# Optimization experiments

Measured on AMD Instinct MI355X. Metric: run time of the kernel, lower is better.

The kernel has to match this reference:

```python
import jax, jax.numpy as jnp
import numpy as np

V, D, N, T, U, E = 200000, 128, 50000, 20, 128, 128

def setup_inputs() -> dict:
    key = jax.random.key(0)
    ks = jax.random.split(key, 12)
    s = 0.02
    return {
        "node_ids": jax.random.randint(ks[0], (N,), 0, V, dtype=jnp.int32),
        "neigh_ids": jax.random.randint(ks[1], (N, T), 0, V, dtype=jnp.int32),
        "alpha": jax.random.uniform(ks[2], (N, T), dtype=jnp.float32),
        "table": jax.random.normal(ks[3], (V, D), dtype=jnp.float32),
        "Wq": jax.random.normal(ks[4], (D, U), dtype=jnp.float32) * s,
        "bq": jnp.zeros((U,), dtype=jnp.float32),
        "Wn": jax.random.normal(ks[5], (D, U), dtype=jnp.float32) * s,
        "bn": jnp.zeros((U,), dtype=jnp.float32),
        "Ww": jax.random.normal(ks[6], (2 * U, U), dtype=jnp.float32) * s,
        "bw": jnp.zeros((U,), dtype=jnp.float32),
        "Wg": jax.random.normal(ks[7], (U, E), dtype=jnp.float32) * s,
        "bg": jnp.zeros((E,), dtype=jnp.float32),
    }

def reference(node_ids, neigh_ids, alpha, table, Wq, bq, Wn, bn, Ww, bw, Wg, bg):
    # gather initial embeddings (irregular indexing)
    node_x = table[node_ids]            # [N, D]
    neigh_x = table[neigh_ids]          # [N, T, D]
    # Convolve: node branch Dense+ReLU
    node_h = jax.nn.relu(node_x @ Wq + bq)                       # [N, U]
    # Aggregator: neighbor Dense+ReLU then alpha-weighted matmul
    neigh_h = jax.nn.relu(jnp.einsum('ntd,du->ntu', neigh_x, Wn) + bn)  # [N, T, U]
    agg = jnp.einsum('nt,ntu->nu', alpha, neigh_h)               # [N, U]
    # concat + Dense+ReLU
    emb = jax.nn.relu(jnp.concatenate([node_h, agg], axis=-1) @ Ww + bw)  # [N, U]
    # global (Frobenius) L2 normalize, as in tf.divide(Emb, tf.norm(Emb, ord=2))
    emb = emb / jnp.linalg.norm(emb)
    # final Dense+ReLU to emb_dim
    return jax.nn.relu(emb @ Wg + bg)                            # [N, E]
```

## Files before the change

kernel.cpp:

```cpp
#include <hip/hip_runtime.h>
#include <math.h>


using f32x4  = __attribute__((ext_vector_type(4))) float;
using short8 = __attribute__((ext_vector_type(8))) short;

typedef const void __attribute__((address_space(1))) gvoid_t;
typedef void       __attribute__((address_space(3))) svoid_t;

__device__ __forceinline__ void gload16(const void* g, void* l) {
    __builtin_amdgcn_global_load_lds((gvoid_t*)g, (svoid_t*)l, 16, 0, 0);
}

__device__ __forceinline__ ushort f2bf(float f) {
    uint u = __float_as_uint(f);
    return (ushort)((u + 0x7fffu + ((u >> 16) & 1u)) >> 16);
}
__device__ __forceinline__ float bf2f(ushort h) {
    return __uint_as_float((uint)h << 16);
}
__device__ __forceinline__ uint pk2(float lo, float hi) {
    return (uint)f2bf(lo) | ((uint)f2bf(hi) << 16);
}
__device__ __forceinline__ short8 pack8(f32x4 a, f32x4 b) {
    uint4 r;
    r.x = pk2(a[0], a[1]); r.y = pk2(a[2], a[3]);
    r.z = pk2(b[0], b[1]); r.w = pk2(b[2], b[3]);
    union { uint4 u; short8 s; } cv; cv.u = r; return cv.s;
}

__global__ __launch_bounds__(256)
void prep_weights(const float* __restrict__ Wq, const float* __restrict__ Wn,
                  const float* __restrict__ Ww, const float* __restrict__ Wg,
                  ushort* __restrict__ WqT, ushort* __restrict__ WnT,
                  ushort* __restrict__ WwT, ushort* __restrict__ WgT)
{
    int idx = blockIdx.x * 256 + threadIdx.x;
    const float* W; ushort* WT; int K; int j = idx;
    if (j < 16384)      { W = Wq; WT = WqT; K = 128; }
    else if (j < 32768) { W = Wn; WT = WnT; K = 128; j -= 16384; }
    else if (j < 65536) { W = Ww; WT = WwT; K = 256; j -= 32768; }
    else                { W = Wg; WT = WgT; K = 128; j -= 65536; }
    int n = j & 127, k = j >> 7;
    WT[(size_t)n * K + k] = f2bf(W[j]);
}

template<bool GATHER>
__device__ __forceinline__ void stage_tile(const float* __restrict__ table,
                                           const int* __restrict__ gidx,
                                           float* Ab, int tile, int M,
                                           int w, int l)
{
#pragma unroll
    for (int j = 0; j < 8; ++j) {
        const int u   = j * 2 + w;
        const int idx = u * 64 + l;
        const int r   = idx >> 5;
        const int c   = idx & 31;
        int grow = tile * 32 + r;
        if (grow > M - 1) grow = M - 1;
        const int g = GATHER ? gidx[grow] : grow;
        const char* src = (const char*)table + (size_t)g * 512
                        + (size_t)((c * 16) ^ ((r & 7) << 4));
        gload16(src, (char*)Ab + u * 1024);
    }
}

__global__ __launch_bounds__(128, 2)
void k1_async(const float* __restrict__ table, const int* __restrict__ node_ids,
              const ushort* __restrict__ WnT, const float* __restrict__ bn,
              const ushort* __restrict__ WqT, const float* __restrict__ bq,
              ushort* __restrict__ H, ushort* __restrict__ nh,
              int V, int N, int splitH)
{
    __shared__ __align__(16) ushort Wlds[128 * 128];
    __shared__ __align__(16) float  Abuf[2][32 * 128];
    __shared__ __align__(16) float  blds[128];
    const int tid = threadIdx.x;
    const int w = tid >> 6, l = tid & 63, l16 = l & 15, lh = l >> 4;
    const bool isH = (int)blockIdx.x < splitH;

    const ushort* WT = isH ? WnT : WqT;
#pragma unroll
    for (int it = 0; it < 16; ++it) {
        int idx = it * 128 + tid, n = idx >> 4, o = idx & 15;
        uint4 v = *reinterpret_cast<const uint4*>(&WT[(size_t)n * 128 + 8 * o]);
        *reinterpret_cast<uint4*>((char*)Wlds + n * 256 + ((16 * o) ^ ((n & 7) << 4))) = v;
    }
    blds[tid] = (isH ? bn : bq)[tid];

    const int M   = isH ? V : N;
    ushort* out   = isH ? H : nh;
    const int ldo = isH ? 128 : 256;
    const int nt  = (M + 31) >> 5;
    const int bidx = isH ? (int)blockIdx.x : (int)blockIdx.x - splitH;
    const int nblk = isH ? splitH : (int)gridDim.x - splitH;

    int tile = bidx;
    if (tile < nt) {
        if (isH) stage_tile<false>(table, nullptr,  Abuf[0], tile, M, w, l);
        else     stage_tile<true >(table, node_ids, Abuf[0], tile, M, w, l);
    }
    __syncthreads();

    int cur = 0;
    const int r = 16 * w + l16;
    for (; tile < nt; tile += nblk) {
        const int nxt = tile + nblk;
        if (nxt < nt) {
            if (isH) stage_tile<false>(table, nullptr,  Abuf[cur ^ 1], nxt, M, w, l);
            else     stage_tile<true >(table, node_ids, Abuf[cur ^ 1], nxt, M, w, l);
        }

        const char* Ab = (const char*)Abuf[cur];
        short8 a[4];
#pragma unroll
        for (int ks = 0; ks < 4; ++ks) {
            f32x4 b0 = *reinterpret_cast<const f32x4*>(
                Ab + r * 512 + ((ks * 128 + lh * 32)      ^ ((r & 7) << 4)));
            f32x4 b1 = *reinterpret_cast<const f32x4*>(
                Ab + r * 512 + ((ks * 128 + lh * 32 + 16) ^ ((r & 7) << 4)));
            a[ks] = pack8(b0, b1);
        }

        f32x4 acc[8];
#pragma unroll
        for (int mt = 0; mt < 8; ++mt)
#pragma unroll
            for (int i = 0; i < 4; ++i) acc[mt][i] = 0.f;
#pragma unroll
        for (int ks = 0; ks < 4; ++ks)
#pragma unroll
            for (int mt = 0; mt < 8; ++mt) {
                short8 wf = *reinterpret_cast<const short8*>(
                    (const char*)Wlds + (16 * mt + l16) * 256 +
                    ((64 * ks + 16 * lh) ^ ((l16 & 7) << 4)));
                acc[mt] = __builtin_amdgcn_mfma_f32_16x16x32_bf16(wf, a[ks], acc[mt], 0, 0, 0);
            }

        const int grow = tile * 32 + r;
        if (grow < M) {
#pragma unroll
            for (int mt = 0; mt < 8; ++mt) {
                f32x4 bv = *reinterpret_cast<const f32x4*>(&blds[16 * mt + 4 * lh]);
                uint2 q;
                q.x = pk2(fmaxf(acc[mt][0] + bv[0], 0.f), fmaxf(acc[mt][1] + bv[1], 0.f));
                q.y = pk2(fmaxf(acc[mt][2] + bv[2], 0.f), fmaxf(acc[mt][3] + bv[3], 0.f));
                *reinterpret_cast<uint2*>(&out[(size_t)grow * ldo + 16 * mt + 4 * lh]) = q;
            }
        }
        __syncthreads();
        cur ^= 1;
    }
}

__global__ __launch_bounds__(256)
void agg_bf16(const ushort* __restrict__ H,
              const int* __restrict__ nids,
              const float* __restrict__ alpha,
              ushort* __restrict__ outb,
              int N)
{
    const int n   = blockIdx.x * 16 + (threadIdx.x >> 4);
    const int l16 = threadIdx.x & 15;
    if (n >= N) return;

    const int*   idp = &nids[n * 20];
    const float* alp = &alpha[n * 20];
    float a[8];
#pragma unroll
    for (int j = 0; j < 8; ++j) a[j] = 0.f;
#pragma unroll
    for (int t = 0; t < 20; ++t) {
        const int   id = idp[t];
        const float al = alp[t];
        uint4 h = *reinterpret_cast<const uint4*>(&H[(size_t)id * 128 + 8 * l16]);
        a[0] = fmaf(al, bf2f((ushort)(h.x & 0xffff)), a[0]);
        a[1] = fmaf(al, bf2f((ushort)(h.x >> 16)),    a[1]);
        a[2] = fmaf(al, bf2f((ushort)(h.y & 0xffff)), a[2]);
        a[3] = fmaf(al, bf2f((ushort)(h.y >> 16)),    a[3]);
        a[4] = fmaf(al, bf2f((ushort)(h.z & 0xffff)), a[4]);
        a[5] = fmaf(al, bf2f((ushort)(h.z >> 16)),    a[5]);
        a[6] = fmaf(al, bf2f((ushort)(h.w & 0xffff)), a[6]);
        a[7] = fmaf(al, bf2f((ushort)(h.w >> 16)),    a[7]);
    }
    uint4 p;
    p.x = pk2(a[0], a[1]); p.y = pk2(a[2], a[3]);
    p.z = pk2(a[4], a[5]); p.w = pk2(a[6], a[7]);
    *reinterpret_cast<uint4*>(&outb[(size_t)n * 256 + 8 * l16]) = p;
}

template<int KTOT, bool GATHER, bool ABF16, bool SUMSQ, bool SCALE, bool OUTBF16>
__global__ __launch_bounds__(256, 2)
void mfma_gemm(const void* __restrict__ Av, int lda,
               const int* __restrict__ gidx,
               const ushort* __restrict__ WT,
               const float* __restrict__ bias,
               void* __restrict__ outv, int ldo, int M,
               float* __restrict__ partials,
               const float* __restrict__ scale_ptr)
{
    __shared__ __align__(16) char smem[65536];
    __shared__ float red[256];
    char* Bbase = smem + 32768;

    const int tid = threadIdx.x;
    const int w   = tid >> 6;
    const int l   = tid & 63;
    const int l16 = l & 15, lh = l >> 4;
    const int brow = blockIdx.x * 128;

    f32x4 acc[2][8];
#pragma unroll
    for (int fr = 0; fr < 2; ++fr)
#pragma unroll
        for (int fc = 0; fc < 8; ++fc)
#pragma unroll
            for (int i = 0; i < 4; ++i) acc[fr][fc][i] = 0.f;

    for (int k0 = 0; k0 < KTOT; k0 += 128) {
        if (ABF16) {
            const ushort* A = (const ushort*)Av;
#pragma unroll
            for (int it = 0; it < 8; ++it) {
                int idx = it * 256 + tid;
                int r = idx >> 4, o = idx & 15;
                int row = brow + r; int grow = (row < M) ? row : (M - 1);
                if (GATHER) grow = gidx[grow];
                uint4 v = *reinterpret_cast<const uint4*>(&A[(size_t)grow * lda + k0 + 8 * o]);
                *reinterpret_cast<uint4*>(smem + r * 256 + ((16 * o) ^ ((r & 7) << 4))) = v;
            }
        } else {
            const float* A = (const float*)Av;
#pragma unroll
            for (int it = 0; it < 16; ++it) {
                int idx = it * 256 + tid;
                int r = idx >> 5, q = idx & 31;
                int row = brow + r; int grow = (row < M) ? row : (M - 1);
                if (GATHER) grow = gidx[grow];
                float4 v = *reinterpret_cast<const float4*>(&A[(size_t)grow * lda + k0 + 4 * q]);
                uint2 p;
                p.x = pk2(v.x, v.y);
                p.y = pk2(v.z, v.w);
                *reinterpret_cast<uint2*>(smem + r * 256 + ((8 * q) ^ ((r & 7) << 4))) = p;
            }
        }
#pragma unroll
        for (int it = 0; it < 8; ++it) {
            int idx = it * 256 + tid;
            int n = idx >> 4, o = idx & 15;
            uint4 v = *reinterpret_cast<const uint4*>(&WT[(size_t)n * KTOT + k0 + 8 * o]);
            *reinterpret_cast<uint4*>(Bbase + n * 256 + ((16 * o) ^ ((n & 7) << 4))) = v;
        }
        __syncthreads();

        const int r0 = 32 * w + l16;
        const int r1 = r0 + 16;
#pragma unroll
        for (int ks = 0; ks < 4; ++ks) {
            const int kb = 64 * ks + 16 * lh;
            short8 a0 = *reinterpret_cast<const short8*>(
                smem + r0 * 256 + (kb ^ ((r0 & 7) << 4)));
            short8 a1 = *reinterpret_cast<const short8*>(
                smem + r1 * 256 + (kb ^ ((r1 & 7) << 4)));
#pragma unroll
            for (int fc = 0; fc < 8; ++fc) {
                const int nn = 16 * fc + l16;
                short8 b = *reinterpret_cast<const short8*>(
                    Bbase + nn * 256 + (kb ^ ((nn & 7) << 4)));
                acc[0][fc] = __builtin_amdgcn_mfma_f32_16x16x32_bf16(a0, b, acc[0][fc], 0, 0, 0);
                acc[1][fc] = __builtin_amdgcn_mfma_f32_16x16x32_bf16(a1, b, acc[1][fc], 0, 0, 0);
            }
        }
        __syncthreads();
    }

    const float scale = SCALE ? scale_ptr[0] : 1.0f;
    float bloc[8];
#pragma unroll
    for (int fc = 0; fc < 8; ++fc) bloc[fc] = bias[16 * fc + l16];

    float ssq = 0.f;
#pragma unroll
    for (int fr = 0; fr < 2; ++fr)
#pragma unroll
        for (int fc = 0; fc < 8; ++fc)
#pragma unroll
            for (int i = 0; i < 4; ++i) {
                const int r   = 32 * w + 16 * fr + 4 * lh + i;
                const int col = 16 * fc + l16;
                float v = fmaxf(fmaf(acc[fr][fc][i], scale, bloc[fc]), 0.f);
                if (SUMSQ) { if (brow + r < M) ssq += v * v; }
                if (OUTBF16) ((ushort*)smem)[r * 128 + col] = f2bf(v);
                else         ((float*)smem)[r * 128 + col] = v;
            }
    __syncthreads();

    if (OUTBF16) {
        ushort* out = (ushort*)outv;
#pragma unroll
        for (int it = 0; it < 8; ++it) {
            int idx = it * 256 + tid;
            int r = idx >> 4, o = idx & 15;
            if (brow + r < M)
                *reinterpret_cast<uint4*>(&out[(size_t)(brow + r) * ldo + 8 * o]) =
                    *reinterpret_cast<const uint4*>((ushort*)smem + r * 128 + 8 * o);
        }
    } else {
        float* out = (float*)outv;
#pragma unroll
        for (int it = 0; it < 16; ++it) {
            int idx = it * 256 + tid;
            int r = idx >> 5, q = idx & 31;
            if (brow + r < M)
                *reinterpret_cast<float4*>(&out[(size_t)(brow + r) * ldo + 4 * q]) =
                    *reinterpret_cast<const float4*>((float*)smem + r * 128 + 4 * q);
        }
    }

    if (SUMSQ) {
        red[tid] = ssq;
        __syncthreads();
        for (int st = 128; st > 0; st >>= 1) {
            if (tid < st) red[tid] += red[tid + st];
            __syncthreads();
        }
        if (tid == 0) partials[blockIdx.x] = red[0];
    }
}

__global__ void reduce_norm(const float* __restrict__ partials, int n,
                            float* __restrict__ scale)
{
    __shared__ float red[256];
    float s = 0.f;
    for (int i = threadIdx.x; i < n; i += 256) s += partials[i];
    red[threadIdx.x] = s;
    __syncthreads();
    for (int st = 128; st > 0; st >>= 1) {
        if (threadIdx.x < st) red[threadIdx.x] += red[threadIdx.x + st];
        __syncthreads();
    }
    if (threadIdx.x == 0) scale[0] = 1.0f / sqrtf(red[0]);
}

extern "C" void kernel_launch(void* const* d_in, const int* in_sizes, int n_in,
                              void* d_out, int out_size, void* d_ws, size_t ws_size,
                              hipStream_t stream)
{
    const int*   node_ids  = (const int*)  d_in[0];
    const int*   neigh_ids = (const int*)  d_in[1];
    const float* alpha     = (const float*)d_in[2];
    const float* table     = (const float*)d_in[3];
    const float* Wq        = (const float*)d_in[4];
    const float* bq        = (const float*)d_in[5];
    const float* Wn        = (const float*)d_in[6];
    const float* bn        = (const float*)d_in[7];
    const float* Ww        = (const float*)d_in[8];
    const float* bw        = (const float*)d_in[9];
    const float* Wg        = (const float*)d_in[10];
    const float* bg        = (const float*)d_in[11];

    const int N = in_sizes[0];
    const int V = in_sizes[3] / 128;
    float* out = (float*)d_out;

    ushort* H    = (ushort*)d_ws;
    ushort* nh   = H    + (size_t)V * 128;
    ushort* embb = nh   + (size_t)N * 256;
    ushort* WqT  = embb + (size_t)N * 128;
    ushort* WnT  = WqT  + 16384;
    ushort* WwT  = WnT  + 16384;
    ushort* WgT  = WwT  + 32768;
    float*  partials = (float*)(WgT + 16384);
    float*  scale    = partials + 512;

    const size_t need = (size_t)((char*)(scale + 16) - (char*)d_ws);
    if (ws_size < need) return;

    const int nblkN = (N + 127) / 128;

    const int G1 = 512;
    const long long tH = (V + 31) / 32, tN = (N + 31) / 32;
    int splitH = (int)((G1 * tH) / (tH + tN));
    if (splitH < 1) splitH = 1;
    if (splitH > G1 - 1) splitH = G1 - 1;

    prep_weights<<<320, 256, 0, stream>>>(Wq, Wn, Ww, Wg, WqT, WnT, WwT, WgT);
    k1_async<<<G1, 128, 0, stream>>>(table, node_ids, WnT, bn, WqT, bq,
                                     H, nh, V, N, splitH);
    agg_bf16<<<(N + 15) / 16, 256, 0, stream>>>(H, neigh_ids, alpha, nh + 128, N);
    mfma_gemm<256, false, true, true, false, true><<<nblkN, 256, 0, stream>>>(
        nh, 256, nullptr, WwT, bw, embb, 128, N, partials, nullptr);
    reduce_norm<<<1, 256, 0, stream>>>(partials, nblkN, scale);
    mfma_gemm<128, false, true, false, true, false><<<nblkN, 256, 0, stream>>>(
        embb, 128, nullptr, WgT, bg, out, 128, N, nullptr, scale);
}
```

Baseline: 112.5 us.

## Restructure first-layer kernel with deep async ring buffer and direct-load gather path

```diff
diff --git a/kernel.cpp b/kernel.cpp
--- a/kernel.cpp
+++ b/kernel.cpp
@@ -11,6 +11,7 @@
 __device__ __forceinline__ void gload16(const void* g, void* l) {
     __builtin_amdgcn_global_load_lds((gvoid_t*)g, (svoid_t*)l, 16, 0, 0);
 }
+#define WAITV(N) asm volatile("s_waitcnt vmcnt(" #N ")" ::: "memory")
 
 __device__ __forceinline__ ushort f2bf(float f) {
     uint u = __float_as_uint(f);
@@ -45,37 +46,16 @@
     WT[(size_t)n * K + k] = f2bf(W[j]);
 }
 
-template<bool GATHER>
-__device__ __forceinline__ void stage_tile(const float* __restrict__ table,
-                                           const int* __restrict__ gidx,
-                                           float* Ab, int tile, int M,
-                                           int w, int l)
-{
-#pragma unroll
-    for (int j = 0; j < 8; ++j) {
-        const int u   = j * 2 + w;
-        const int idx = u * 64 + l;
-        const int r   = idx >> 5;
-        const int c   = idx & 31;
-        int grow = tile * 32 + r;
-        if (grow > M - 1) grow = M - 1;
-        const int g = GATHER ? gidx[grow] : grow;
-        const char* src = (const char*)table + (size_t)g * 512
-                        + (size_t)((c * 16) ^ ((r & 7) << 4));
-        gload16(src, (char*)Ab + u * 1024);
-    }
-}
-
 __global__ __launch_bounds__(128, 2)
-void k1_async(const float* __restrict__ table, const int* __restrict__ node_ids,
-              const ushort* __restrict__ WnT, const float* __restrict__ bn,
-              const ushort* __restrict__ WqT, const float* __restrict__ bq,
-              ushort* __restrict__ H, ushort* __restrict__ nh,
-              int V, int N, int splitH)
-{
-    __shared__ __align__(16) ushort Wlds[128 * 128];
-    __shared__ __align__(16) float  Abuf[2][32 * 128];
-    __shared__ __align__(16) float  blds[128];
+void k1_mix(const float* __restrict__ table, const int* __restrict__ node_ids,
+            const ushort* __restrict__ WnT, const float* __restrict__ bn,
+            const ushort* __restrict__ WqT, const float* __restrict__ bq,
+            ushort* __restrict__ H, ushort* __restrict__ nh,
+            int V, int N, int splitH)
+{
+    __shared__ __align__(16) char Wlds[32768];
+    __shared__ __align__(16) char Abuf[5 * 8192];
+    __shared__ __align__(16) float blds[128];
     const int tid = threadIdx.x;
     const int w = tid >> 6, l = tid & 63, l16 = l & 15, lh = l >> 4;
     const bool isH = (int)blockIdx.x < splitH;
@@ -83,74 +63,141 @@
     const ushort* WT = isH ? WnT : WqT;
 #pragma unroll
     for (int it = 0; it < 16; ++it) {
-        int idx = it * 128 + tid, n = idx >> 4, o = idx & 15;
-        uint4 v = *reinterpret_cast<const uint4*>(&WT[(size_t)n * 128 + 8 * o]);
-        *reinterpret_cast<uint4*>((char*)Wlds + n * 256 + ((16 * o) ^ ((n & 7) << 4))) = v;
+        int c = it * 128 + tid;
+        int mtks = c >> 6, lane = c & 63;
+        const ushort* src = WT + (size_t)(16 * (mtks >> 2) + (lane & 15)) * 128
+                          + 32 * (mtks & 3) + 8 * (lane >> 4);
+        *reinterpret_cast<uint4*>(Wlds + (size_t)c * 16) =
+            *reinterpret_cast<const uint4*>(src);
     }
     blds[tid] = (isH ? bn : bq)[tid];
 
-    const int M   = isH ? V : N;
-    ushort* out   = isH ? H : nh;
-    const int ldo = isH ? 128 : 256;
-    const int nt  = (M + 31) >> 5;
-    const int bidx = isH ? (int)blockIdx.x : (int)blockIdx.x - splitH;
-    const int nblk = isH ? splitH : (int)gridDim.x - splitH;
-
-    int tile = bidx;
-    if (tile < nt) {
-        if (isH) stage_tile<false>(table, nullptr,  Abuf[0], tile, M, w, l);
-        else     stage_tile<true >(table, node_ids, Abuf[0], tile, M, w, l);
-    }
-    __syncthreads();
-
-    int cur = 0;
-    const int r = 16 * w + l16;
-    for (; tile < nt; tile += nblk) {
-        const int nxt = tile + nblk;
-        if (nxt < nt) {
-            if (isH) stage_tile<false>(table, nullptr,  Abuf[cur ^ 1], nxt, M, w, l);
-            else     stage_tile<true >(table, node_ids, Abuf[cur ^ 1], nxt, M, w, l);
-        }
-
-        const char* Ab = (const char*)Abuf[cur];
-        short8 a[4];
-#pragma unroll
-        for (int ks = 0; ks < 4; ++ks) {
-            f32x4 b0 = *reinterpret_cast<const f32x4*>(
-                Ab + r * 512 + ((ks * 128 + lh * 32)      ^ ((r & 7) << 4)));
-            f32x4 b1 = *reinterpret_cast<const f32x4*>(
-                Ab + r * 512 + ((ks * 128 + lh * 32 + 16) ^ ((r & 7) << 4)));
-            a[ks] = pack8(b0, b1);
-        }
-
-        f32x4 acc[8];
-#pragma unroll
-        for (int mt = 0; mt < 8; ++mt)
-#pragma unroll
-            for (int i = 0; i < 4; ++i) acc[mt][i] = 0.f;
-#pragma unroll
-        for (int ks = 0; ks < 4; ++ks)
-#pragma unroll
-            for (int mt = 0; mt < 8; ++mt) {
-                short8 wf = *reinterpret_cast<const short8*>(
-                    (const char*)Wlds + (16 * mt + l16) * 256 +
-                    ((64 * ks + 16 * lh) ^ ((l16 & 7) << 4)));
-                acc[mt] = __builtin_amdgcn_mfma_f32_16x16x32_bf16(wf, a[ks], acc[mt], 0, 0, 0);
-            }
-
-        const int grow = tile * 32 + r;
-        if (grow < M) {
-#pragma unroll
-            for (int mt = 0; mt < 8; ++mt) {
-                f32x4 bv = *reinterpret_cast<const f32x4*>(&blds[16 * mt + 4 * lh]);
-                uint2 q;
-                q.x = pk2(fmaxf(acc[mt][0] + bv[0], 0.f), fmaxf(acc[mt][1] + bv[1], 0.f));
-                q.y = pk2(fmaxf(acc[mt][2] + bv[2], 0.f), fmaxf(acc[mt][3] + bv[3], 0.f));
-                *reinterpret_cast<uint2*>(&out[(size_t)grow * ldo + 16 * mt + 4 * lh]) = q;
-            }
-        }
+    if (isH) {
+        const int M = V, nt = (M + 15) >> 4, ldo = 128;
+        ushort* out = H;
+        const int wid = (int)blockIdx.x, nblk = splitH;
+
+#pragma unroll
+        for (int p = 0; p < 4; ++p) {
+            int tt = wid + p * nblk; if (tt >= nt) tt = wid;
+            int row = tt * 16 + l16; if (row > M - 1) row = M - 1;
+            const char* base = (const char*)table + (size_t)row * 512 + 32 * lh;
+            char* buf = Abuf + p * 8192;
+#pragma unroll
+            for (int j = 0; j < 4; ++j) {
+                int u = 4 * w + j;
+                gload16(base + 128 * (u >> 1) + 16 * (u & 1), buf + u * 1024);
+            }
+        }
+        asm volatile("s_waitcnt lgkmcnt(0)" ::: "memory");
+
+        int i = 0;
+        for (int tile = wid; tile < nt; tile += nblk, ++i) {
+            if (i == 0)      WAITV(12);
+            else if (i == 1) WAITV(16);
+            else if (i == 2) WAITV(20);
+            else if (i == 3) WAITV(24);
+            else             WAITV(28);
+            __builtin_amdgcn_s_barrier();
+            __builtin_amdgcn_sched_barrier(0);
+
+            {
+                int tt = tile + 4 * nblk; if (tt >= nt) tt = tile;
+                int row = tt * 16 + l16; if (row > M - 1) row = M - 1;
+                const char* base = (const char*)table + (size_t)row * 512 + 32 * lh;
+                char* buf = Abuf + ((i + 4) % 5) * 8192;
+#pragma unroll
+                for (int j = 0; j < 4; ++j) {
+                    int u = 4 * w + j;
+                    gload16(base + 128 * (u >> 1) + 16 * (u & 1), buf + u * 1024);
+                }
+            }
+            __builtin_amdgcn_sched_barrier(0);
+
+            const char* Ab = Abuf + (i % 5) * 8192;
+            short8 a[4];
+#pragma unroll
+            for (int ks = 0; ks < 4; ++ks) {
+                f32x4 c0 = *reinterpret_cast<const f32x4*>(Ab + (2 * ks) * 1024 + l * 16);
+                f32x4 c1 = *reinterpret_cast<const f32x4*>(Ab + (2 * ks + 1) * 1024 + l * 16);
+                a[ks] = pack8(c0, c1);
+            }
+            f32x4 acc[4];
+#pragma unroll
+            for (int j = 0; j < 4; ++j)
+#pragma unroll
+                for (int q = 0; q < 4; ++q) acc[j][q] = 0.f;
+#pragma unroll
+            for (int ks = 0; ks < 4; ++ks)
+#pragma unroll
+                for (int j = 0; j < 4; ++j) {
+                    int mt = 4 * w + j;
+                    short8 wf = *reinterpret_cast<const short8*>(
+                        Wlds + (size_t)((mt * 4 + ks) * 64 + l) * 16);
+                    acc[j] = __builtin_amdgcn_mfma_f32_16x16x32_bf16(wf, a[ks], acc[j], 0, 0, 0);
+                }
+
+            const int row = tile * 16 + l16;
+            if (row < M) {
+#pragma unroll
+                for (int j = 0; j < 4; ++j) {
+                    int mt = 4 * w + j;
+                    f32x4 bv = *reinterpret_cast<const f32x4*>(&blds[16 * mt + 4 * lh]);
+                    uint2 q;
+                    q.x = pk2(fmaxf(acc[j][0] + bv[0], 0.f), fmaxf(acc[j][1] + bv[1], 0.f));
+                    q.y = pk2(fmaxf(acc[j][2] + bv[2], 0.f), fmaxf(acc[j][3] + bv[3], 0.f));
+                    *reinterpret_cast<uint2*>(&out[(size_t)row * ldo + 16 * mt + 4 * lh]) = q;
+                }
+            }
+        }
+    } else {
         __syncthreads();
-        cur ^= 1;
+        const int M = N, nt = (M + 15) >> 4, ldo = 256;
+        ushort* out = nh;
+        const int wid = ((int)blockIdx.x - splitH) * 2 + w;
+        const int nwv = ((int)gridDim.x - splitH) * 2;
+
+        for (int tile = wid; tile < nt; tile += nwv) {
+            const int row = tile * 16 + l16;
+            int g = (row < M) ? row : (M - 1);
+            g = node_ids[g];
+            const float* rp = table + (size_t)g * 128 + 8 * lh;
+
+            f32x4 f[8];
+#pragma unroll
+            for (int ks = 0; ks < 4; ++ks) {
+                f[2 * ks]     = *reinterpret_cast<const f32x4*>(rp + 32 * ks);
+                f[2 * ks + 1] = *reinterpret_cast<const f32x4*>(rp + 32 * ks + 4);
+            }
+            short8 a[4];
+#pragma unroll
+            for (int ks = 0; ks < 4; ++ks) a[ks] = pack8(f[2 * ks], f[2 * ks + 1]);
+
+            f32x4 acc[8];
+#pragma unroll
+            for (int mt = 0; mt < 8; ++mt)
+#pragma unroll
+                for (int q = 0; q < 4; ++q) acc[mt][q] = 0.f;
+#pragma unroll
+            for (int ks = 0; ks < 4; ++ks)
+#pragma unroll
+                for (int mt = 0; mt < 8; ++mt) {
+                    short8 wf = *reinterpret_cast<const short8*>(
+                        Wlds + (size_t)((mt * 4 + ks) * 64 + l) * 16);
+                    acc[mt] = __builtin_amdgcn_mfma_f32_16x16x32_bf16(wf, a[ks], acc[mt], 0, 0, 0);
+                }
+
+            if (row < M) {
+#pragma unroll
+                for (int mt = 0; mt < 8; ++mt) {
+                    f32x4 bv = *reinterpret_cast<const f32x4*>(&blds[16 * mt + 4 * lh]);
+                    uint2 q;
+                    q.x = pk2(fmaxf(acc[mt][0] + bv[0], 0.f), fmaxf(acc[mt][1] + bv[1], 0.f));
+                    q.y = pk2(fmaxf(acc[mt][2] + bv[2], 0.f), fmaxf(acc[mt][3] + bv[3], 0.f));
+                    *reinterpret_cast<uint2*>(&out[(size_t)row * ldo + 16 * mt + 4 * lh]) = q;
+                }
+            }
+        }
     }
 }
 
@@ -381,14 +428,14 @@
     const int nblkN = (N + 127) / 128;
 
     const int G1 = 512;
-    const long long tH = (V + 31) / 32, tN = (N + 31) / 32;
-    int splitH = (int)((G1 * tH) / (tH + tN));
+    const long long tH = (V + 15) / 16, tN = (N + 15) / 16;
+    int splitH = (int)(((long long)G1 * tH * 10) / (tH * 10 + tN * 14));
     if (splitH < 1) splitH = 1;
     if (splitH > G1 - 1) splitH = G1 - 1;
 
     prep_weights<<<320, 256, 0, stream>>>(Wq, Wn, Ww, Wg, WqT, WnT, WwT, WgT);
-    k1_async<<<G1, 128, 0, stream>>>(table, node_ids, WnT, bn, WqT, bq,
-                                     H, nh, V, N, splitH);
+    k1_mix<<<G1, 128, 0, stream>>>(table, node_ids, WnT, bn, WqT, bq,
+                                   H, nh, V, N, splitH);
     agg_bf16<<<(N + 15) / 16, 256, 0, stream>>>(H, neigh_ids, alpha, nh + 128, N);
     mfma_gemm<256, false, true, true, false, true><<<nblkN, 256, 0, stream>>>(
         nh, 256, nullptr, WwT, bw, embb, 128, N, partials, nullptr);
```

Result: slower. 118.7 us (+5.5%).
